# Kernel optimization log

Hardware: AMD Instinct MI355X
Metric: run time of the kernel (lower is better)

Reference implementation:

```python
import jax, jax.numpy as jnp
import numpy as np

B, N, C, H = 4, 2048, 384, 6
D = C // H                       # head_dim = 64
HID = 4 * C                      # mlp hidden = 1536
SCALE = D ** -0.5
EPS = 1e-5                       # torch nn.LayerNorm default


def setup_inputs() -> dict:
    key = jax.random.key(0)
    ks = jax.random.split(key, 8)
    s = 0.02
    return {
        "x": jax.random.normal(ks[0], (B, N, C), jnp.float32),
        "ln1_g": jnp.ones((C,), jnp.float32),
        "ln1_b": jnp.zeros((C,), jnp.float32),
        "w_qkv": jax.random.normal(ks[1], (3 * C, C), jnp.float32) * s,
        "w_proj": jax.random.normal(ks[2], (C, C), jnp.float32) * s,
        "b_proj": jnp.zeros((C,), jnp.float32),
        "ln2_g": jnp.ones((C,), jnp.float32),
        "ln2_b": jnp.zeros((C,), jnp.float32),
        "w_fc1": jax.random.normal(ks[3], (HID, C), jnp.float32) * s,
        "b_fc1": jnp.zeros((HID,), jnp.float32),
        "w_fc2": jax.random.normal(ks[4], (C, HID), jnp.float32) * s,
        "b_fc2": jnp.zeros((C,), jnp.float32),
    }


def _layernorm(x, g, b):
    mu = jnp.mean(x, axis=-1, keepdims=True)
    var = jnp.mean(jnp.square(x - mu), axis=-1, keepdims=True)
    return (x - mu) * jax.lax.rsqrt(var + EPS) * g + b


def _bf16_round(x):
    # emulate the .bfloat16() cast after each residual (precision truncation)
    return x.astype(jnp.bfloat16).astype(jnp.float32)


def reference(x, ln1_g, ln1_b, w_qkv, w_proj, b_proj,
              ln2_g, ln2_b, w_fc1, b_fc1, w_fc2, b_fc2):
    # ---- attention branch (quant=False => HMQ ops are pass-through) ----
    h = _layernorm(x, ln1_g, ln1_b)                       # [B,N,C]
    qkv = jnp.einsum('bnc,oc->bno', h, w_qkv)             # [B,N,3C]
    qkv = qkv.reshape(B, N, 3, H, D).transpose(2, 0, 3, 1, 4)  # [3,B,H,N,D]
    q, k, v = qkv[0], qkv[1], qkv[2]
    attn = jnp.einsum('bhnd,bhmd->bhnm', q, k) * SCALE    # [B,H,N,N]
    attn = jax.nn.softmax(attn, axis=-1)
    o = jnp.einsum('bhnm,bhmd->bhnd', attn, v)            # [B,H,N,D]
    o = o.transpose(0, 2, 1, 3).reshape(B, N, C)
    o = jnp.einsum('bnc,oc->bno', o, w_proj) + b_proj
    x = _bf16_round(x + o)

    # ---- MLP branch ----
    h = _layernorm(x, ln2_g, ln2_b)
    h = jnp.einsum('bnc,hc->bnh', h, w_fc1) + b_fc1       # [B,N,HID]
    h = jax.nn.gelu(h, approximate=False)
    h = jnp.einsum('bnh,ch->bnc', h, w_fc2) + b_fc2       # [B,N,C]
    x = _bf16_round(x + h)
    return x
```

## Files before the change

### kernel.cpp

```cpp
#include <hip/hip_runtime.h>
#include <cstdint>
#include <cstddef>

#define DI __device__ __forceinline__

typedef __attribute__((ext_vector_type(8))) short short8;
typedef __attribute__((ext_vector_type(4))) float f32x4;
typedef unsigned int u32;
typedef unsigned short u16;

DI u16 rne_bf16(float f) {
  union { float f; u32 u; } v; v.f = f;
  u32 b = v.u;
  return (u16)((b + 0x7fffu + ((b >> 16) & 1u)) >> 16);
}
DI float bf2f(u16 h) {
  union { u32 u; float f; } v; v.u = ((u32)h) << 16;
  return v.f;
}

DI void gl2lds16(const void* g, void* l) {
  __builtin_amdgcn_global_load_lds(
      (const __attribute__((address_space(1))) u32*)g,
      (__attribute__((address_space(3))) u32*)l, 16, 0, 0);
}

template<int ROWS>
DI void stage_swz(const u16* src, int ld, char* ldsb, int tid) {
  int wbase = tid & ~63;
  #pragma unroll
  for (int c = 0; c < (ROWS * 8) / 256; ++c) {
    int g = c * 256 + tid;
    int row = g >> 3;
    int sgr = (g & 7) ^ (row & 7);
    gl2lds16(src + row * ld + sgr * 8, ldsb + (size_t)(c * 256 + wbase) * 16);
  }
}

DI short8 lds_frag(const char* base, int row, int k0) {
  return *(const short8*)(base + row * 128 + ((k0 * 2) ^ ((row & 7) << 4)));
}

DI f32x4 mfma16(short8 a, short8 b, f32x4 c) {
  return __builtin_amdgcn_mfma_f32_16x16x32_bf16(a, b, c, 0, 0, 0);
}

__global__ __launch_bounds__(256) void cvt_w(
    const float* __restrict__ a, const float* __restrict__ b,
    const float* __restrict__ c, const float* __restrict__ d,
    u16* __restrict__ oa, u16* __restrict__ ob, u16* __restrict__ oc,
    u16* __restrict__ od) {
  int i = blockIdx.x * 256 + threadIdx.x;
  if (i < 442368) oa[i] = rne_bf16(a[i]);
  else if (i < 589824) ob[i - 442368] = rne_bf16(b[i - 442368]);
  else if (i < 1179648) oc[i - 589824] = rne_bf16(c[i - 589824]);
  else if (i < 1769472) od[i - 1179648] = rne_bf16(d[i - 1179648]);
}

template<int INBF>
__global__ __launch_bounds__(256) void ln_k(
    const void* __restrict__ xin, const float* __restrict__ gam,
    const float* __restrict__ bet, u16* __restrict__ out) {
  int row = blockIdx.x * 4 + (threadIdx.x >> 6);
  int lane = threadIdx.x & 63;
  float v[6];
  if (INBF) {
    const u16* x = (const u16*)xin + (size_t)row * 384 + lane * 6;
    #pragma unroll
    for (int j = 0; j < 6; ++j) v[j] = bf2f(x[j]);
  } else {
    const float* x = (const float*)xin + (size_t)row * 384 + lane * 6;
    #pragma unroll
    for (int j = 0; j < 6; ++j) v[j] = x[j];
  }
  float s = 0.f;
  #pragma unroll
  for (int j = 0; j < 6; ++j) s += v[j];
  #pragma unroll
  for (int d = 1; d < 64; d <<= 1) s += __shfl_xor(s, d);
  float mu = s * (1.f / 384.f);
  float q = 0.f;
  #pragma unroll
  for (int j = 0; j < 6; ++j) { float t = v[j] - mu; q += t * t; }
  #pragma unroll
  for (int d = 1; d < 64; d <<= 1) q += __shfl_xor(q, d);
  float rstd = rsqrtf(q * (1.f / 384.f) + 1e-5f);
  #pragma unroll
  for (int j = 0; j < 6; ++j) {
    int c = lane * 6 + j;
    out[(size_t)row * 384 + c] = rne_bf16((v[j] - mu) * rstd * gam[c] + bet[c]);
  }
}

struct EpiP {
  const float* bias;
  const float* residf;
  const u16* residb;
  u16* outb;
  float* outf;
  u16* q; u16* k; u16* v;
};

template<int EPI>
__global__ __launch_bounds__(256) void gemm_bt(
    const u16* __restrict__ A, const u16* __restrict__ W, int K, EpiP p) {
  __shared__ char lds[65536];
  int tid = threadIdx.x, lane = tid & 63, wid = tid >> 6;
  int wr = wid >> 1, wc = wid & 1;
  int fr = lane & 15, k8 = lane >> 4;
  int bm = blockIdx.x, bn = blockIdx.y;
  const u16* Ab = A + (size_t)bm * 128 * K;
  const u16* Wb = W + (size_t)bn * 128 * K;

  stage_swz<128>(Ab, K, lds, tid);
  stage_swz<128>(Wb, K, lds + 16384, tid);

  f32x4 zz = {0.f, 0.f, 0.f, 0.f};
  f32x4 acc[4][4];
  #pragma unroll
  for (int mr = 0; mr < 4; ++mr)
    #pragma unroll
    for (int nc = 0; nc < 4; ++nc) acc[mr][nc] = zz;

  asm volatile("s_waitcnt vmcnt(0)" ::: "memory");
  __syncthreads();

  int KT = K >> 6;
  for (int t = 0; t < KT; ++t) {
    char* base = lds + (size_t)(t & 1) * 32768;
    if (t + 1 < KT) {
      char* nb = lds + (size_t)((t + 1) & 1) * 32768;
      stage_swz<128>(Ab + (t + 1) * 64, K, nb, tid);
      stage_swz<128>(Wb + (t + 1) * 64, K, nb + 16384, tid);
    }
    #pragma unroll
    for (int ks = 0; ks < 2; ++ks) {
      int k0 = ks * 32 + k8 * 8;
      short8 av[4], bv[4];
      #pragma unroll
      for (int mr = 0; mr < 4; ++mr) av[mr] = lds_frag(base, wr * 64 + mr * 16 + fr, k0);
      #pragma unroll
      for (int nc = 0; nc < 4; ++nc) bv[nc] = lds_frag(base + 16384, wc * 64 + nc * 16 + fr, k0);
      #pragma unroll
      for (int mr = 0; mr < 4; ++mr)
        #pragma unroll
        for (int nc = 0; nc < 4; ++nc)
          acc[mr][nc] = mfma16(av[mr], bv[nc], acc[mr][nc]);
    }
    asm volatile("s_waitcnt vmcnt(0)" ::: "memory");
    __syncthreads();
  }

  #pragma unroll
  for (int mr = 0; mr < 4; ++mr)
    #pragma unroll
    for (int nc = 0; nc < 4; ++nc)
      #pragma unroll
      for (int r = 0; r < 4; ++r) {
        int m = bm * 128 + wr * 64 + mr * 16 + k8 * 4 + r;
        int o = bn * 128 + wc * 64 + nc * 16 + fr;
        float val = acc[mr][nc][r];
        if constexpr (EPI == 0) {
          int tq = o / 384;
          int rem = o - tq * 384;
          int hh = rem >> 6, d = rem & 63;
          int b = m >> 11, n = m & 2047;
          u16 bvs = rne_bf16(val);
          size_t qk = (((size_t)(b * 6 + hh)) * 2048 + n) * 64 + d;
          if (tq == 0) p.q[qk] = bvs;
          else if (tq == 1) p.k[qk] = bvs;
          else p.v[qk] = bvs;
        } else if constexpr (EPI == 1) {
          size_t idx = (size_t)m * 384 + o;
          float r2 = p.residf[idx] + val + p.bias[o];
          p.outb[idx] = rne_bf16(r2);
        } else if constexpr (EPI == 2) {
          size_t idx = (size_t)m * 1536 + o;
          float z = val + p.bias[o];
          float gl = 0.5f * z * (1.f + erff(z * 0.70710678118654752f));
          p.outb[idx] = rne_bf16(gl);
        } else {
          size_t idx = (size_t)m * 384 + o;
          float r2 = bf2f(p.residb[idx]) + val + p.bias[o];
          p.outf[idx] = bf2f(rne_bf16(r2));
        }
      }
}

__global__ __launch_bounds__(256) void vtr_k(
    const u16* __restrict__ v, u16* __restrict__ vt) {
  __shared__ u16 t[64 * 72];
  int tid = threadIdx.x;
  int n0 = blockIdx.x * 64, bh = blockIdx.y;
  const u16* src = v + ((size_t)bh * 2048 + n0) * 64;
  #pragma unroll
  for (int it = 0; it < 2; ++it) {
    int row = it * 32 + (tid >> 3), c8 = tid & 7;
    *(short8*)&t[row * 72 + c8 * 8] = *(const short8*)(src + row * 64 + c8 * 8);
  }
  __syncthreads();
  int d = tid & 63, c = tid >> 6;
  u16 o[16];
  #pragma unroll
  for (int j = 0; j < 16; ++j) o[j] = t[(c * 16 + j) * 72 + d];
  u16* dst = vt + ((size_t)bh * 64 + d) * 2048 + n0 + c * 16;
  *(short8*)dst = *(short8*)&o[0];
  *(short8*)(dst + 8) = *(short8*)&o[8];
}

__global__ __launch_bounds__(256) void attn_k(
    const u16* __restrict__ Qg, const u16* __restrict__ Kg,
    const u16* __restrict__ Vg, float* __restrict__ Op, float* __restrict__ lp) {
  __shared__ char lds[51712];
  int tid = threadIdx.x, lane = tid & 63, wid = tid >> 6;
  int fr = lane & 15, k8 = lane >> 4;
  int qt = blockIdx.x, bh = blockIdx.y, z = blockIdx.z;
  const u16* Qb = Qg + (size_t)bh * 2048 * 64;
  const u16* Kb = Kg + ((size_t)bh * 2048 + z * 1024) * 64;
  const u16* Vb = Vg + (size_t)bh * 64 * 2048 + z * 1024;
  int qr0 = qt * 128 + wid * 32;

  short8 qf[2][2];
  #pragma unroll
  for (int mr = 0; mr < 2; ++mr)
    #pragma unroll
    for (int ks = 0; ks < 2; ++ks)
      qf[mr][ks] = *(const short8*)(Qb + (size_t)(qr0 + mr * 16 + fr) * 64 + ks * 32 + k8 * 8);

  f32x4 zz = {0.f, 0.f, 0.f, 0.f};
  f32x4 oacc[2][4];
  float lrun[2][4];
  #pragma unroll
  for (int mr = 0; mr < 2; ++mr) {
    #pragma unroll
    for (int nc = 0; nc < 4; ++nc) oacc[mr][nc] = zz;
    #pragma unroll
    for (int r = 0; r < 4; ++r) lrun[mr][r] = 0.f;
  }
  char* P = lds + 32768 + wid * 4736;

  stage_swz<64>(Kb, 64, lds, tid);
  stage_swz<64>(Vb, 2048, lds + 16384, tid);
  asm volatile("s_waitcnt vmcnt(0)" ::: "memory");
  __syncthreads();

  for (int t = 0; t < 16; ++t) {
    char* kbase = lds + (size_t)(t & 1) * 8192;
    char* vbase = lds + 16384 + (size_t)(t & 1) * 8192;
    if (t < 15) {
      stage_swz<64>(Kb + (size_t)(t + 1) * 64 * 64, 64, lds + (size_t)((t + 1) & 1) * 8192, tid);
      stage_swz<64>(Vb + (t + 1) * 64, 2048, lds + 16384 + (size_t)((t + 1) & 1) * 8192, tid);
    }
    f32x4 s[2][4];
    #pragma unroll
    for (int mr = 0; mr < 2; ++mr)
      #pragma unroll
      for (int nc = 0; nc < 4; ++nc) s[mr][nc] = zz;
    #pragma unroll
    for (int ks = 0; ks < 2; ++ks) {
      int k0 = ks * 32 + k8 * 8;
      short8 kf[4];
      #pragma unroll
      for (int nc = 0; nc < 4; ++nc) kf[nc] = lds_frag(kbase, nc * 16 + fr, k0);
      __builtin_amdgcn_s_setprio(1);
      #pragma unroll
      for (int mr = 0; mr < 2; ++mr)
        #pragma unroll
        for (int nc = 0; nc < 4; ++nc)
          s[mr][nc] = mfma16(qf[mr][ks], kf[nc], s[mr][nc]);
      __builtin_amdgcn_s_setprio(0);
    }
    #pragma unroll
    for (int mr = 0; mr < 2; ++mr)
      #pragma unroll
      for (int nc = 0; nc < 4; ++nc)
        #pragma unroll
        for (int r = 0; r < 4; ++r) {
          float pv = __expf(s[mr][nc][r] * 0.125f);
          lrun[mr][r] += pv;
          ((u16*)P)[(mr * 16 + k8 * 4 + r) * 74 + nc * 16 + fr] = rne_bf16(pv);
        }
    #pragma unroll
    for (int ks = 0; ks < 2; ++ks) {
      int k0 = ks * 32 + k8 * 8;
      short8 pa[2], vf[4];
      #pragma unroll
      for (int mr = 0; mr < 2; ++mr)
        pa[mr] = *(const short8*)(P + (mr * 16 + fr) * 148 + k0 * 2);
      #pragma unroll
      for (int nc = 0; nc < 4; ++nc) vf[nc] = lds_frag(vbase, nc * 16 + fr, k0);
      __builtin_amdgcn_s_setprio(1);
      #pragma unroll
      for (int mr = 0; mr < 2; ++mr)
        #pragma unroll
        for (int nc = 0; nc < 4; ++nc)
          oacc[mr][nc] = mfma16(pa[mr], vf[nc], oacc[mr][nc]);
      __builtin_amdgcn_s_setprio(0);
    }
    asm volatile("s_waitcnt vmcnt(0)" ::: "memory");
    __syncthreads();
  }

  #pragma unroll
  for (int mr = 0; mr < 2; ++mr)
    #pragma unroll
    for (int r = 0; r < 4; ++r) {
      float t2 = lrun[mr][r];
      #pragma unroll
      for (int dd = 1; dd < 16; dd <<= 1) t2 += __shfl_xor(t2, dd);
      lrun[mr][r] = t2;
    }
  size_t rowb = (size_t)z * 49152 + (size_t)bh * 2048;
  #pragma unroll
  for (int mr = 0; mr < 2; ++mr)
    #pragma unroll
    for (int nc = 0; nc < 4; ++nc)
      #pragma unroll
      for (int r = 0; r < 4; ++r) {
        int qrow = qr0 + mr * 16 + k8 * 4 + r;
        Op[(rowb + qrow) * 64 + nc * 16 + fr] = oacc[mr][nc][r];
      }
  if (fr == 0)
    #pragma unroll
    for (int mr = 0; mr < 2; ++mr)
      #pragma unroll
      for (int r = 0; r < 4; ++r)
        lp[rowb + qr0 + mr * 16 + k8 * 4 + r] = lrun[mr][r];
}

__global__ __launch_bounds__(256) void attn_merge(
    const float* __restrict__ Op, const float* __restrict__ lp,
    u16* __restrict__ ao) {
  int row = blockIdx.x * 4 + (threadIdx.x >> 6);
  int d = threadIdx.x & 63;
  float l = lp[row] + lp[49152 + row];
  float v = (Op[(size_t)row * 64 + d] + Op[(size_t)(49152 + row) * 64 + d]) / l;
  int bh = row >> 11, n = row & 2047;
  int b = bh / 6, hh = bh - b * 6;
  ao[((size_t)(b * 2048 + n)) * 384 + hh * 64 + d] = rne_bf16(v);
}

extern "C" void kernel_launch(void* const* d_in, const int* in_sizes, int n_in,
                              void* d_out, int out_size, void* d_ws, size_t ws_size,
                              hipStream_t stream) {
  const float* x     = (const float*)d_in[0];
  const float* ln1g  = (const float*)d_in[1];
  const float* ln1b  = (const float*)d_in[2];
  const float* wqkv  = (const float*)d_in[3];
  const float* wproj = (const float*)d_in[4];
  const float* bproj = (const float*)d_in[5];
  const float* ln2g  = (const float*)d_in[6];
  const float* ln2b  = (const float*)d_in[7];
  const float* wfc1  = (const float*)d_in[8];
  const float* bfc1  = (const float*)d_in[9];
  const float* wfc2  = (const float*)d_in[10];
  const float* bfc2  = (const float*)d_in[11];
  float* out = (float*)d_out;

  char* w = (char*)d_ws;
  u16* h1     = (u16*)w; w += 6291456;
  u16* x2     = (u16*)w; w += 6291456;
  u16* h2     = (u16*)w; w += 6291456;
  u16* qb     = (u16*)w; w += 6291456;
  u16* kb     = (u16*)w; w += 6291456;
  u16* vtb    = (u16*)w; w += 6291456;
  u16* ao     = (u16*)w; w += 6291456;
  u16* act    = (u16*)w; w += 25165824;
  u16* wqkvb  = (u16*)w; w += 884736;
  u16* wprojb = (u16*)w; w += 294912;
  u16* wfc1b  = (u16*)w; w += 1179648;
  u16* wfc2b  = (u16*)w; w += 1179648;

  u16* v_nat   = h2;
  float* Opart = (float*)act;
  float* lpart = (float*)h2;

  cvt_w<<<6912, 256, 0, stream>>>(wqkv, wproj, wfc1, wfc2, wqkvb, wprojb, wfc1b, wfc2b);
  ln_k<0><<<2048, 256, 0, stream>>>(x, ln1g, ln1b, h1);
  {
    EpiP p{}; p.q = qb; p.k = kb; p.v = v_nat;
    gemm_bt<0><<<dim3(64, 9), 256, 0, stream>>>(h1, wqkvb, 384, p);
  }
  vtr_k<<<dim3(32, 24), 256, 0, stream>>>(v_nat, vtb);
  attn_k<<<dim3(16, 24, 2), 256, 0, stream>>>(qb, kb, vtb, Opart, lpart);
  attn_merge<<<12288, 256, 0, stream>>>(Opart, lpart, ao);
  {
    EpiP p{}; p.bias = bproj; p.residf = x; p.outb = x2;
    gemm_bt<1><<<dim3(64, 3), 256, 0, stream>>>(ao, wprojb, 384, p);
  }
  ln_k<1><<<2048, 256, 0, stream>>>(x2, ln2g, ln2b, h2);
  {
    EpiP p{}; p.bias = bfc1; p.outb = act;
    gemm_bt<2><<<dim3(64, 12), 256, 0, stream>>>(h2, wfc1b, 384, p);
  }
  {
    EpiP p{}; p.bias = bfc2; p.residb = x2; p.outf = out;
    gemm_bt<3><<<dim3(64, 3), 256, 0, stream>>>(act, wfc2b, 1536, p);
  }
}
```

Before: 252.2 us.

## Triple-buffer attention K/V loads, swizzle P tile, and shrink GEMM M-tiles

The attention kernel moves from a double-buffered to a triple-buffered K/V LDS pipeline. It issues loads two tiles ahead and waits with a partial vmcnt and a raw s_barrier instead of a full drain and __syncthreads. The P scratch tile now uses an XOR-swizzled 128-byte-row layout instead of padded rows, and exp uses exp2f with a folded scale. The GEMM is templated on M-tile size so that the QKV, proj and fc2 GEMMs run with 64-row tiles and twice as many blocks, giving better CU fill; the cost is less reuse of each staged W tile.

```diff
diff --git a/kernel.cpp b/kernel.cpp
--- a/kernel.cpp
+++ b/kernel.cpp
@@ -23,6 +23,12 @@
   __builtin_amdgcn_global_load_lds(
       (const __attribute__((address_space(1))) u32*)g,
       (__attribute__((address_space(3))) u32*)l, 16, 0, 0);
+}
+
+DI void bar() {
+  asm volatile("" ::: "memory");
+  __builtin_amdgcn_s_barrier();
+  asm volatile("" ::: "memory");
 }
 
 template<int ROWS>
@@ -101,50 +107,53 @@
   u16* q; u16* k; u16* v;
 };
 
-template<int EPI>
+template<int EPI, int MT>
 __global__ __launch_bounds__(256) void gemm_bt(
     const u16* __restrict__ A, const u16* __restrict__ W, int K, EpiP p) {
-  __shared__ char lds[65536];
+  constexpr int ABUF = MT * 128;
+  constexpr int NC = (MT == 128) ? 4 : 2;
+  __shared__ char lds[2 * (ABUF + 16384)];
   int tid = threadIdx.x, lane = tid & 63, wid = tid >> 6;
-  int wr = wid >> 1, wc = wid & 1;
+  int wr = (MT == 128) ? (wid >> 1) * 64 : 0;
+  int wcb = (MT == 128) ? (wid & 1) * 64 : wid * 32;
   int fr = lane & 15, k8 = lane >> 4;
   int bm = blockIdx.x, bn = blockIdx.y;
-  const u16* Ab = A + (size_t)bm * 128 * K;
+  const u16* Ab = A + (size_t)bm * MT * K;
   const u16* Wb = W + (size_t)bn * 128 * K;
 
-  stage_swz<128>(Ab, K, lds, tid);
-  stage_swz<128>(Wb, K, lds + 16384, tid);
+  stage_swz<MT>(Ab, K, lds, tid);
+  stage_swz<128>(Wb, K, lds + ABUF, tid);
 
   f32x4 zz = {0.f, 0.f, 0.f, 0.f};
-  f32x4 acc[4][4];
+  f32x4 acc[4][NC];
   #pragma unroll
   for (int mr = 0; mr < 4; ++mr)
     #pragma unroll
-    for (int nc = 0; nc < 4; ++nc) acc[mr][nc] = zz;
+    for (int nc = 0; nc < NC; ++nc) acc[mr][nc] = zz;
 
   asm volatile("s_waitcnt vmcnt(0)" ::: "memory");
   __syncthreads();
 
   int KT = K >> 6;
   for (int t = 0; t < KT; ++t) {
-    char* base = lds + (size_t)(t & 1) * 32768;
+    char* base = lds + (size_t)(t & 1) * (ABUF + 16384);
     if (t + 1 < KT) {
-      char* nb = lds + (size_t)((t + 1) & 1) * 32768;
-      stage_swz<128>(Ab + (t + 1) * 64, K, nb, tid);
-      stage_swz<128>(Wb + (t + 1) * 64, K, nb + 16384, tid);
+      char* nb = lds + (size_t)((t + 1) & 1) * (ABUF + 16384);
+      stage_swz<MT>(Ab + (t + 1) * 64, K, nb, tid);
+      stage_swz<128>(Wb + (t + 1) * 64, K, nb + ABUF, tid);
     }
     #pragma unroll
     for (int ks = 0; ks < 2; ++ks) {
       int k0 = ks * 32 + k8 * 8;
-      short8 av[4], bv[4];
-      #pragma unroll
-      for (int mr = 0; mr < 4; ++mr) av[mr] = lds_frag(base, wr * 64 + mr * 16 + fr, k0);
-      #pragma unroll
-      for (int nc = 0; nc < 4; ++nc) bv[nc] = lds_frag(base + 16384, wc * 64 + nc * 16 + fr, k0);
+      short8 av[4], bv[NC];
+      #pragma unroll
+      for (int mr = 0; mr < 4; ++mr) av[mr] = lds_frag(base, wr + mr * 16 + fr, k0);
+      #pragma unroll
+      for (int nc = 0; nc < NC; ++nc) bv[nc] = lds_frag(base + ABUF, wcb + nc * 16 + fr, k0);
       #pragma unroll
       for (int mr = 0; mr < 4; ++mr)
         #pragma unroll
-        for (int nc = 0; nc < 4; ++nc)
+        for (int nc = 0; nc < NC; ++nc)
           acc[mr][nc] = mfma16(av[mr], bv[nc], acc[mr][nc]);
     }
     asm volatile("s_waitcnt vmcnt(0)" ::: "memory");
@@ -154,11 +163,11 @@
   #pragma unroll
   for (int mr = 0; mr < 4; ++mr)
     #pragma unroll
-    for (int nc = 0; nc < 4; ++nc)
+    for (int nc = 0; nc < NC; ++nc)
       #pragma unroll
       for (int r = 0; r < 4; ++r) {
-        int m = bm * 128 + wr * 64 + mr * 16 + k8 * 4 + r;
-        int o = bn * 128 + wc * 64 + nc * 16 + fr;
+        int m = bm * MT + wr + mr * 16 + k8 * 4 + r;
+        int o = bn * 128 + wcb + nc * 16 + fr;
         float val = acc[mr][nc][r];
         if constexpr (EPI == 0) {
           int tq = o / 384;
@@ -211,7 +220,7 @@
 __global__ __launch_bounds__(256) void attn_k(
     const u16* __restrict__ Qg, const u16* __restrict__ Kg,
     const u16* __restrict__ Vg, float* __restrict__ Op, float* __restrict__ lp) {
-  __shared__ char lds[51712];
+  __shared__ char lds[65536];
   int tid = threadIdx.x, lane = tid & 63, wid = tid >> 6;
   int fr = lane & 15, k8 = lane >> 4;
   int qt = blockIdx.x, bh = blockIdx.y, z = blockIdx.z;
@@ -237,20 +246,21 @@
     #pragma unroll
     for (int r = 0; r < 4; ++r) lrun[mr][r] = 0.f;
   }
-  char* P = lds + 32768 + wid * 4736;
-
-  stage_swz<64>(Kb, 64, lds, tid);
-  stage_swz<64>(Vb, 2048, lds + 16384, tid);
-  asm volatile("s_waitcnt vmcnt(0)" ::: "memory");
-  __syncthreads();
+  char* P = lds + 49152 + wid * 4096;
+
+  #define STAGE(t)                                                            \
+    stage_swz<64>(Kb + (size_t)(t) * 64 * 64, 64, lds + ((t) % 3) * 8192, tid); \
+    stage_swz<64>(Vb + (t) * 64, 2048, lds + 24576 + ((t) % 3) * 8192, tid);
+
+  STAGE(0);
+  STAGE(1);
+  asm volatile("s_waitcnt vmcnt(4)" ::: "memory");
+  bar();
 
   for (int t = 0; t < 16; ++t) {
-    char* kbase = lds + (size_t)(t & 1) * 8192;
-    char* vbase = lds + 16384 + (size_t)(t & 1) * 8192;
-    if (t < 15) {
-      stage_swz<64>(Kb + (size_t)(t + 1) * 64 * 64, 64, lds + (size_t)((t + 1) & 1) * 8192, tid);
-      stage_swz<64>(Vb + (t + 1) * 64, 2048, lds + 16384 + (size_t)((t + 1) & 1) * 8192, tid);
-    }
+    if (t + 2 < 16) { STAGE(t + 2); }
+    char* kbase = lds + (t % 3) * 8192;
+    char* vbase = lds + 24576 + (t % 3) * 8192;
     f32x4 s[2][4];
     #pragma unroll
     for (int mr = 0; mr < 2; ++mr)
@@ -276,9 +286,11 @@
       for (int nc = 0; nc < 4; ++nc)
         #pragma unroll
         for (int r = 0; r < 4; ++r) {
-          float pv = __expf(s[mr][nc][r] * 0.125f);
+          float pv = exp2f(s[mr][nc][r] * 0.18033688011112042f);
           lrun[mr][r] += pv;
-          ((u16*)P)[(mr * 16 + k8 * 4 + r) * 74 + nc * 16 + fr] = rne_bf16(pv);
+          int row7 = (k8 * 4 + r) & 7;
+          *(u16*)(P + (mr * 16 + k8 * 4 + r) * 128 +
+                  (((nc * 16 + fr) * 2) ^ (row7 << 4))) = rne_bf16(pv);
         }
     #pragma unroll
     for (int ks = 0; ks < 2; ++ks) {
@@ -286,7 +298,8 @@
       short8 pa[2], vf[4];
       #pragma unroll
       for (int mr = 0; mr < 2; ++mr)
-        pa[mr] = *(const short8*)(P + (mr * 16 + fr) * 148 + k0 * 2);
+        pa[mr] = *(const short8*)(P + (mr * 16 + fr) * 128 +
+                                  ((k0 * 2) ^ ((fr & 7) << 4)));
       #pragma unroll
       for (int nc = 0; nc < 4; ++nc) vf[nc] = lds_frag(vbase, nc * 16 + fr, k0);
       __builtin_amdgcn_s_setprio(1);
@@ -297,9 +310,11 @@
           oacc[mr][nc] = mfma16(pa[mr], vf[nc], oacc[mr][nc]);
       __builtin_amdgcn_s_setprio(0);
     }
-    asm volatile("s_waitcnt vmcnt(0)" ::: "memory");
-    __syncthreads();
-  }
+    if (t <= 13) { asm volatile("s_waitcnt vmcnt(4)" ::: "memory"); }
+    else if (t == 14) { asm volatile("s_waitcnt vmcnt(0)" ::: "memory"); }
+    if (t < 15) bar();
+  }
+  #undef STAGE
 
   #pragma unroll
   for (int mr = 0; mr < 2; ++mr)
@@ -379,22 +394,22 @@
   ln_k<0><<<2048, 256, 0, stream>>>(x, ln1g, ln1b, h1);
   {
     EpiP p{}; p.q = qb; p.k = kb; p.v = v_nat;
-    gemm_bt<0><<<dim3(64, 9), 256, 0, stream>>>(h1, wqkvb, 384, p);
+    gemm_bt<0, 64><<<dim3(128, 9), 256, 0, stream>>>(h1, wqkvb, 384, p);
   }
   vtr_k<<<dim3(32, 24), 256, 0, stream>>>(v_nat, vtb);
   attn_k<<<dim3(16, 24, 2), 256, 0, stream>>>(qb, kb, vtb, Opart, lpart);
   attn_merge<<<12288, 256, 0, stream>>>(Opart, lpart, ao);
   {
     EpiP p{}; p.bias = bproj; p.residf = x; p.outb = x2;
-    gemm_bt<1><<<dim3(64, 3), 256, 0, stream>>>(ao, wprojb, 384, p);
+    gemm_bt<1, 64><<<dim3(128, 3), 256, 0, stream>>>(ao, wprojb, 384, p);
   }
   ln_k<1><<<2048, 256, 0, stream>>>(x2, ln2g, ln2b, h2);
   {
     EpiP p{}; p.bias = bfc1; p.outb = act;
-    gemm_bt<2><<<dim3(64, 12), 256, 0, stream>>>(h2, wfc1b, 384, p);
+    gemm_bt<2, 128><<<dim3(64, 12), 256, 0, stream>>>(h2, wfc1b, 384, p);
   }
   {
     EpiP p{}; p.bias = bfc2; p.residb = x2; p.outf = out;
-    gemm_bt<3><<<dim3(64, 3), 256, 0, stream>>>(act, wfc2b, 1536, p);
-  }
-}
+    gemm_bt<3, 64><<<dim3(128, 3), 256, 0, stream>>>(act, wfc2b, 1536, p);
+  }
+}
```

Result: no change. 247.5 us (-1.9%).
